# Performance work log

Measured on AMD Instinct MI355X. Metric: run time of the kernel, lower is better.

The kernel has to match this reference:

```python
import jax, jax.numpy as jnp
from jax import lax
import numpy as np

B, S, D = 64, 512, 768
W = 256          # number of words per sentence (counts sum <= S since counts in {1,2})
H = 384          # lstm_dim
C = 425          # n_classes


def setup_inputs() -> dict:
    key = jax.random.key(0)
    ks = jax.random.split(key, 12)
    sc_ih = 1.0 / np.sqrt(D)
    sc_hh = 1.0 / np.sqrt(H)
    return {
        "f0": jax.random.normal(ks[0], (B, S, D), dtype=jnp.float32),
        "counts": jax.random.randint(ks[1], (B, W), 1, 3, dtype=jnp.int32),  # pieces per word in {1,2}
        "Wih_f": jax.random.normal(ks[2], (4 * H, D), dtype=jnp.float32) * sc_ih,
        "Whh_f": jax.random.normal(ks[3], (4 * H, H), dtype=jnp.float32) * sc_hh,
        "bih_f": jax.random.normal(ks[4], (4 * H,), dtype=jnp.float32) * sc_hh,
        "bhh_f": jax.random.normal(ks[5], (4 * H,), dtype=jnp.float32) * sc_hh,
        "Wih_b": jax.random.normal(ks[6], (4 * H, D), dtype=jnp.float32) * sc_ih,
        "Whh_b": jax.random.normal(ks[7], (4 * H, H), dtype=jnp.float32) * sc_hh,
        "bih_b": jax.random.normal(ks[8], (4 * H,), dtype=jnp.float32) * sc_hh,
        "bhh_b": jax.random.normal(ks[9], (4 * H,), dtype=jnp.float32) * sc_hh,
        "Wlin": jax.random.normal(ks[10], (C, 2 * H), dtype=jnp.float32) * (1.0 / np.sqrt(2 * H)),
        "blin": jax.random.normal(ks[11], (C,), dtype=jnp.float32) * 0.02,
    }


def segment_mean_pool(f0, counts):
    # Ragged segment-mean: word j in sentence i pools wordpieces [start, start+counts) .
    starts = jnp.cumsum(counts, axis=1) - counts          # [B, W] start offset per word
    total = jnp.sum(counts, axis=1)                       # [B] total wordpieces used
    pos = jnp.arange(S)
    # segment id of each wordpiece position: number of starts <= pos, minus 1
    seg = jnp.sum(starts[:, :, None] <= pos[None, None, :], axis=1) - 1   # [B, S]
    valid = pos[None, :] < total[:, None]
    seg = jnp.where(valid, seg, W)                        # route padding into dump segment W
    sums = jax.vmap(lambda f, s: jax.ops.segment_sum(f, s, num_segments=W + 1))(f0, seg)  # [B, W+1, D]
    pooled = sums[:, :W] / counts[..., None].astype(f0.dtype)
    # Original writes means into positions [0, W) in-place; tail [W, S) keeps raw states.
    return f0.at[:, :W].set(pooled)


def lstm_dir(x, Wih, Whh, bih, bhh, reverse):
    # x: [B, S, D]; PyTorch gate order i, f, g, o
    xp = jnp.einsum('bsd,gd->bsg', x, Wih) + bih + bhh    # precompute input projections

    def step(carry, xt):
        h, c = carry
        gates = xt + h @ Whh.T
        i, f, g, o = jnp.split(gates, 4, axis=-1)
        c = jax.nn.sigmoid(f) * c + jax.nn.sigmoid(i) * jnp.tanh(g)
        h = jax.nn.sigmoid(o) * jnp.tanh(c)
        return (h, c), h

    init = (jnp.zeros((x.shape[0], H), x.dtype), jnp.zeros((x.shape[0], H), x.dtype))
    _, hs = lax.scan(step, init, jnp.swapaxes(xp, 0, 1), reverse=reverse)  # [S, B, H]
    return jnp.swapaxes(hs, 0, 1)


def reference(f0, counts, Wih_f, Whh_f, bih_f, bhh_f, Wih_b, Whh_b, bih_b, bhh_b, Wlin, blin):
    f0 = segment_mean_pool(f0, counts)
    hf = lstm_dir(f0, Wih_f, Whh_f, bih_f, bhh_f, reverse=False)
    hb = lstm_dir(f0, Wih_b, Whh_b, bih_b, bhh_b, reverse=True)
    f1 = jnp.concatenate([hf, hb], axis=-1)               # [B, S, 2H]
    # Linear then dropout (eval mode -> identity)
    return jnp.einsum('bsh,ch->bsc', f1, Wlin) + blin
```

## Files before the change

### kernel.cpp

```cpp
#include <hip/hip_runtime.h>
#include <stdint.h>


typedef __attribute__((ext_vector_type(8))) short short8;
typedef __attribute__((ext_vector_type(4))) float f32x4;

static constexpr int Bn = 64, Sn = 512, Dn = 768, Wn = 256, Hn = 384, Cn = 425;
static constexpr int G4H = 4 * Hn;
static constexpr int NBT = 4;
static constexpr int NCK = 6;

__device__ __forceinline__ unsigned short f2bf(float f) {
  unsigned int u = __float_as_uint(f);
  u += 0x7FFFu + ((u >> 16) & 1u);
  return (unsigned short)(u >> 16);
}
__device__ __forceinline__ float bf2f(unsigned short h) {
  return __uint_as_float(((unsigned int)h) << 16);
}
__device__ __forceinline__ float sigm(float x)  { return 1.f / (1.f + __expf(-x)); }
__device__ __forceinline__ float tanhft(float x){ return 1.f - 2.f / (__expf(2.f * x) + 1.f); }

#define GLL16(gp, lp) __builtin_amdgcn_global_load_lds( \
  (const __attribute__((address_space(1))) unsigned int*)(gp), \
  (__attribute__((address_space(3))) unsigned int*)(lp), 16, 0, 0)

__global__ void zero_comm(unsigned int* p, int nwords) {
  int i = blockIdx.x * 256 + threadIdx.x;
  if (i < nwords)
    __hip_atomic_store(&p[i], 0u, __ATOMIC_RELAXED, __HIP_MEMORY_SCOPE_AGENT);
}

__global__ void scan_starts(const int* __restrict__ counts, int* __restrict__ starts) {
  int b = blockIdx.x, j = threadIdx.x;
  __shared__ int sm[256];
  int c = counts[b * Wn + j];
  sm[j] = c;
  __syncthreads();
  for (int off = 1; off < 256; off <<= 1) {
    int v = (j >= off) ? sm[j - off] : 0;
    __syncthreads();
    sm[j] += v;
    __syncthreads();
  }
  starts[b * Wn + j] = sm[j] - c;
}

__global__ void prep_cast(const float* __restrict__ Wih_f, const float* __restrict__ Wih_b,
                          const float* __restrict__ Whh_f, const float* __restrict__ Whh_b,
                          const float* __restrict__ Wlin,
                          const float* __restrict__ bih_f, const float* __restrict__ bhh_f,
                          const float* __restrict__ bih_b, const float* __restrict__ bhh_b,
                          unsigned short* __restrict__ wih, unsigned short* __restrict__ whh,
                          unsigned short* __restrict__ wlin, float* __restrict__ biasc) {
  int i = blockIdx.x * 256 + threadIdx.x;
  const int T0 = 3072 * 768;
  const int T1 = 2 * 1536 * 384;
  const int T2 = Cn * 768;
  const int T3 = 3072;
  if (i < T0) {
    int n = i / 768, k = i - n * 768;
    float v = (n < 1536) ? Wih_f[n * 768 + k] : Wih_b[(n - 1536) * 768 + k];
    wih[i] = f2bf(v);
  } else if (i < T0 + T1) {
    int j = i - T0;
    float v = (j < 1536 * 384) ? Whh_f[j] : Whh_b[j - 1536 * 384];
    whh[j] = f2bf(v);
  } else if (i < T0 + T1 + T2) {
    int j = i - T0 - T1;
    wlin[j] = f2bf(Wlin[j]);
  } else if (i < T0 + T1 + T2 + T3) {
    int n = i - T0 - T1 - T2;
    biasc[n] = (n < 1536) ? (bih_f[n] + bhh_f[n]) : (bih_b[n - 1536] + bhh_b[n - 1536]);
  }
}

__global__ void pool_kernel(const float* __restrict__ f0, const int* __restrict__ counts,
                            const int* __restrict__ starts, unsigned short* __restrict__ f0p) {
  int idx = blockIdx.x * 256 + threadIdx.x;
  int dc = idx % 192;
  int rest = idx / 192;
  int s = rest & 511, b = rest >> 9;
  const float4* f4 = (const float4*)f0;
  float4 v;
  if (s < Wn) {
    int st = starts[b * Wn + s], cnt = counts[b * Wn + s];
    v = f4[(size_t)(b * Sn + st) * 192 + dc];
    if (cnt == 2) {
      float4 v2 = f4[(size_t)(b * Sn + st + 1) * 192 + dc];
      v.x = (v.x + v2.x) * 0.5f; v.y = (v.y + v2.y) * 0.5f;
      v.z = (v.z + v2.z) * 0.5f; v.w = (v.w + v2.w) * 0.5f;
    }
  } else {
    v = f4[(size_t)(b * Sn + s) * 192 + dc];
  }
  ushort4 o;
  o.x = f2bf(v.x); o.y = f2bf(v.y); o.z = f2bf(v.z); o.w = f2bf(v.w);
  ((ushort4*)f0p)[(size_t)(b * Sn + s) * 192 + dc] = o;
}

__global__ void gemm_xp(const unsigned short* __restrict__ A, const unsigned short* __restrict__ Bw,
                        const float* __restrict__ biasc, unsigned short* __restrict__ xp) {
  __shared__ __align__(16) unsigned short As[128 * 32];
  __shared__ __align__(16) unsigned short Bs[128 * 32];
  int tid = threadIdx.x, w = tid >> 6, l = tid & 63, lr = l & 15, lq = l >> 4;
  int mBase = blockIdx.x * 128, nBase = blockIdx.y * 128;
  int mw = (w & 1) * 64, nw = (w >> 1) * 64;
  f32x4 acc[4][4];
#pragma unroll
  for (int mt = 0; mt < 4; ++mt)
#pragma unroll
    for (int nt = 0; nt < 4; ++nt) acc[mt][nt] = (f32x4){0.f, 0.f, 0.f, 0.f};

  for (int kb = 0; kb < 24; ++kb) {
    int k0 = kb * 32;
#pragma unroll
    for (int j = 0; j < 2; ++j) {
      int g = j * 256 + tid;
      int row = g >> 2, kc = (g & 3) * 8;
      GLL16(A + (size_t)(mBase + row) * 768 + k0 + kc, (char*)As + (j * 256 + w * 64) * 16);
      GLL16(Bw + (size_t)(nBase + row) * 768 + k0 + kc, (char*)Bs + (j * 256 + w * 64) * 16);
    }
    __syncthreads();
    short8 af[4], bfv[4];
#pragma unroll
    for (int mt = 0; mt < 4; ++mt) af[mt] = *(const short8*)&As[(mw + mt * 16 + lr) * 32 + lq * 8];
#pragma unroll
    for (int nt = 0; nt < 4; ++nt) bfv[nt] = *(const short8*)&Bs[(nw + nt * 16 + lr) * 32 + lq * 8];
#pragma unroll
    for (int mt = 0; mt < 4; ++mt)
#pragma unroll
      for (int nt = 0; nt < 4; ++nt)
        acc[mt][nt] = __builtin_amdgcn_mfma_f32_16x16x32_bf16(af[mt], bfv[nt], acc[mt][nt], 0, 0, 0);
    __syncthreads();
  }
#pragma unroll
  for (int nt = 0; nt < 4; ++nt) {
    int n = nBase + nw + nt * 16 + lr;
    float bias = biasc[n];
    int d = (n >= 1536) ? 1 : 0;
    int gI = n - d * 1536;
#pragma unroll
    for (int mt = 0; mt < 4; ++mt) {
      int mrow = mBase + mw + mt * 16 + lq * 4;
#pragma unroll
      for (int r = 0; r < 4; ++r) {
        int m = mrow + r;
        int t = m & 511, b = m >> 9;
        xp[((size_t)((d * Sn + t) * Bn + b)) * 1536 + gI] = f2bf(acc[mt][nt][r] + bias);
      }
    }
  }
}

__global__ void __launch_bounds__(256, 1)
recur_kernel(const unsigned short* __restrict__ whh,
             const unsigned short* __restrict__ xp,
             unsigned short* __restrict__ h_all,
             unsigned int* __restrict__ htag) {
  int bid = blockIdx.x;
  int dir = bid / (NBT * NCK);
  int rem = bid % (NBT * NCK);
  int btile = rem / NCK, chunk = rem % NCK;
  int tid = threadIdx.x, w = tid >> 6, l = tid & 63, lr = l & 15, lq = l >> 4;
  int hwb = chunk * 64 + w * 16;
  int pr = tid >> 4, pk = tid & 15;

  __shared__ __align__(16) unsigned int hlds[2][16 * 196];

  short8 bfr[4][12];
#pragma unroll
  for (int q = 0; q < 4; ++q)
#pragma unroll
    for (int kf = 0; kf < 12; ++kf)
      bfr[q][kf] = *(const short8*)&whh[((size_t)dir * 1536 + q * 384 + hwb + lr) * 384 + kf * 32 + lq * 8];

  f32x4 c0 = (f32x4){0.f, 0.f, 0.f, 0.f};

  for (int it = 0; it < Sn; ++it) {
    int t = dir ? (Sn - 1 - it) : it;

    f32x4 acc[4];
#pragma unroll
    for (int q = 0; q < 4; ++q) {
#pragma unroll
      for (int r = 0; r < 4; ++r) {
        int b = btile * 16 + lq * 4 + r;
        acc[q][r] = bf2f(xp[((size_t)((dir * Sn + t) * Bn + b)) * 1536 + q * 384 + hwb + lr]);
      }
    }

    if (it > 0) {
      const unsigned int expT = (unsigned int)it;
      int slot = (it - 1) & 1;
      const unsigned long long* srow = (const unsigned long long*)
          (htag + (size_t)(dir * 2 + slot) * 64 * 384 + (size_t)(btile * 16 + pr) * 384);
      unsigned long long v[12];
      while (true) {
        bool ok = true;
#pragma unroll
        for (int i = 0; i < 12; ++i) {
          unsigned long long x = __hip_atomic_load(&srow[pk + 16 * i],
                                   __ATOMIC_RELAXED, __HIP_MEMORY_SCOPE_AGENT);
          v[i] = x;
          ok &= (((unsigned int)(x >> 16) & 0xffffu) == expT) &
                ((unsigned int)(x >> 48) == expT);
        }
        if (__all((int)ok)) break;
        __builtin_amdgcn_s_sleep(1);
      }
      unsigned int* dst = hlds[it & 1];
#pragma unroll
      for (int i = 0; i < 12; ++i)
        dst[pr * 196 + pk + 16 * i] = ((unsigned int)v[i] & 0xffffu) |
                                      (((unsigned int)(v[i] >> 32) & 0xffffu) << 16);
      __syncthreads();
      const char* src = (const char*)hlds[it & 1];
#pragma unroll
      for (int kf = 0; kf < 12; ++kf) {
        short8 a = *(const short8*)(src + lr * 784 + kf * 64 + lq * 16);
#pragma unroll
        for (int q = 0; q < 4; ++q)
          acc[q] = __builtin_amdgcn_mfma_f32_16x16x32_bf16(a, bfr[q][kf], acc[q], 0, 0, 0);
      }
    }

    unsigned int outTag = (unsigned int)(it + 1) << 16;
    int oslot = it & 1;
    unsigned int* obase = htag + (size_t)(dir * 2 + oslot) * 64 * 384;
    unsigned short hb16v[4];
#pragma unroll
    for (int r = 0; r < 4; ++r) {
      float iv = sigm(acc[0][r]);
      float fv = sigm(acc[1][r]);
      float gv = tanhft(acc[2][r]);
      float ov = sigm(acc[3][r]);
      float cf = fv * c0[r] + iv * gv;
      c0[r] = cf;
      float hv = ov * tanhft(cf);
      hb16v[r] = f2bf(hv);
      int b = btile * 16 + lq * 4 + r;
      __hip_atomic_store(&obase[(size_t)b * 384 + hwb + lr],
                         outTag | hb16v[r], __ATOMIC_RELAXED, __HIP_MEMORY_SCOPE_AGENT);
    }
#pragma unroll
    for (int r = 0; r < 4; ++r) {
      int b = btile * 16 + lq * 4 + r;
      h_all[((size_t)b * Sn + t) * 768 + dir * Hn + hwb + lr] = hb16v[r];
    }
  }
}

__global__ void gemm_out(const unsigned short* __restrict__ A, const unsigned short* __restrict__ Bw,
                         const float* __restrict__ blin, float* __restrict__ out) {
  __shared__ __align__(16) unsigned short As[128 * 32];
  __shared__ __align__(16) unsigned short Bs[128 * 32];
  int tid = threadIdx.x, w = tid >> 6, l = tid & 63, lr = l & 15, lq = l >> 4;
  int mBase = blockIdx.x * 128, nBase = blockIdx.y * 128;
  int mw = (w & 1) * 64, nw = (w >> 1) * 64;
  f32x4 acc[4][4];
#pragma unroll
  for (int mt = 0; mt < 4; ++mt)
#pragma unroll
    for (int nt = 0; nt < 4; ++nt) acc[mt][nt] = (f32x4){0.f, 0.f, 0.f, 0.f};

  for (int kb = 0; kb < 24; ++kb) {
    int k0 = kb * 32;
#pragma unroll
    for (int j = 0; j < 2; ++j) {
      int g = j * 256 + tid;
      int row = g >> 2, kc = (g & 3) * 8;
      int nr = nBase + row; if (nr > Cn - 1) nr = Cn - 1;
      GLL16(A + (size_t)(mBase + row) * 768 + k0 + kc, (char*)As + (j * 256 + w * 64) * 16);
      GLL16(Bw + (size_t)nr * 768 + k0 + kc, (char*)Bs + (j * 256 + w * 64) * 16);
    }
    __syncthreads();
    short8 af[4], bfv[4];
#pragma unroll
    for (int mt = 0; mt < 4; ++mt) af[mt] = *(const short8*)&As[(mw + mt * 16 + lr) * 32 + lq * 8];
#pragma unroll
    for (int nt = 0; nt < 4; ++nt) bfv[nt] = *(const short8*)&Bs[(nw + nt * 16 + lr) * 32 + lq * 8];
#pragma unroll
    for (int mt = 0; mt < 4; ++mt)
#pragma unroll
      for (int nt = 0; nt < 4; ++nt)
        acc[mt][nt] = __builtin_amdgcn_mfma_f32_16x16x32_bf16(af[mt], bfv[nt], acc[mt][nt], 0, 0, 0);
    __syncthreads();
  }
#pragma unroll
  for (int nt = 0; nt < 4; ++nt) {
    int n = nBase + nw + nt * 16 + lr;
    if (n < Cn) {
      float bias = blin[n];
#pragma unroll
      for (int mt = 0; mt < 4; ++mt) {
        int mrow = mBase + mw + mt * 16 + lq * 4;
#pragma unroll
        for (int r = 0; r < 4; ++r) {
          int m = mrow + r;
          out[(size_t)m * Cn + n] = acc[mt][nt][r] + bias;
        }
      }
    }
  }
}

extern "C" void kernel_launch(void* const* d_in, const int* in_sizes, int n_in,
                              void* d_out, int out_size, void* d_ws, size_t ws_size,
                              hipStream_t stream) {
  (void)in_sizes; (void)n_in; (void)out_size;
  const float* f0     = (const float*)d_in[0];
  const int*   counts = (const int*)  d_in[1];
  const float* Wih_f  = (const float*)d_in[2];
  const float* Whh_f  = (const float*)d_in[3];
  const float* bih_f  = (const float*)d_in[4];
  const float* bhh_f  = (const float*)d_in[5];
  const float* Wih_b  = (const float*)d_in[6];
  const float* Whh_b  = (const float*)d_in[7];
  const float* bih_b  = (const float*)d_in[8];
  const float* bhh_b  = (const float*)d_in[9];
  const float* Wlin   = (const float*)d_in[10];
  const float* blin   = (const float*)d_in[11];
  float* out = (float*)d_out;

  char* ws = (char*)d_ws;
  size_t o = 0;
  auto alloc = [&](size_t bytes) { size_t cur = o; o += (bytes + 255) & ~(size_t)255; return cur; };
  size_t o_f0p    = alloc((size_t)Bn * Sn * Dn * 2);
  size_t o_xp     = alloc((size_t)2 * Sn * Bn * G4H * 2);
  size_t o_wih    = alloc((size_t)3072 * 768 * 2);
  size_t o_whh    = alloc((size_t)2 * 1536 * 384 * 2);
  size_t o_wlin   = alloc((size_t)Cn * 768 * 2);
  size_t o_bias   = alloc((size_t)3072 * 4);
  size_t o_starts = alloc((size_t)Bn * Wn * 4);
  size_t o_htag   = alloc((size_t)2 * 2 * 64 * 384 * 4);
  if (o > ws_size) return;

  unsigned short* f0p   = (unsigned short*)(ws + o_f0p);
  unsigned short* h_all = (unsigned short*)(ws + o_f0p);
  unsigned short* xp    = (unsigned short*)(ws + o_xp);
  unsigned short* wih   = (unsigned short*)(ws + o_wih);
  unsigned short* whh   = (unsigned short*)(ws + o_whh);
  unsigned short* wlin  = (unsigned short*)(ws + o_wlin);
  float*          biasc = (float*)(ws + o_bias);
  int*            starts= (int*)(ws + o_starts);
  unsigned int*   htag  = (unsigned int*)(ws + o_htag);

  {
    int nwords = 2 * 2 * 64 * 384;
    zero_comm<<<(nwords + 255) / 256, 256, 0, stream>>>(htag, nwords);
  }
  scan_starts<<<Bn, 256, 0, stream>>>(counts, starts);
  {
    int total = 3072 * 768 + 2 * 1536 * 384 + Cn * 768 + 3072;
    prep_cast<<<(total + 255) / 256, 256, 0, stream>>>(Wih_f, Wih_b, Whh_f, Whh_b, Wlin,
                                                       bih_f, bhh_f, bih_b, bhh_b,
                                                       wih, whh, wlin, biasc);
  }
  pool_kernel<<<(Bn * Sn * 192) / 256, 256, 0, stream>>>(f0, counts, starts, f0p);
  gemm_xp<<<dim3(256, 24), 256, 0, stream>>>(f0p, wih, biasc, xp);
  recur_kernel<<<2 * NBT * NCK, 256, 0, stream>>>(whh, xp, h_all, htag);
  gemm_out<<<dim3(256, 4), 256, 0, stream>>>(h_all, wlin, blin, out);
}
```

Baseline: 1.889 ms.

## Exchange LSTM hidden state through XCD-local buffers with runtime XCD detection

The recurrence kernel now launches 64 blocks and maps them so that each group of six chunk-blocks sharing a batch tile and direction can detect whether they all landed on the same XCD. When they did, hidden states are exchanged through a per-XCD buffer using sc0 loads and stores, so the polling traffic can stay in the XCD-local cache instead of going to device-coherent memory. A bounded spin falls back to the original agent-scope tagged buffer, which is still always written. The change also prefetches the next step's input projections into registers to hide load latency, and swizzles the LDS layout to reduce bank conflicts. The XCD-local path relies on the hardware scheduler's block-to-XCD placement and on cache-coherence behaviour. It adds setup handshakes and duplicate stores.

```diff
diff --git a/kernel.cpp b/kernel.cpp
--- a/kernel.cpp
+++ b/kernel.cpp
@@ -4,11 +4,13 @@
 
 typedef __attribute__((ext_vector_type(8))) short short8;
 typedef __attribute__((ext_vector_type(4))) float f32x4;
+typedef __attribute__((ext_vector_type(4))) unsigned int u32x4;
 
 static constexpr int Bn = 64, Sn = 512, Dn = 768, Wn = 256, Hn = 384, Cn = 425;
 static constexpr int G4H = 4 * Hn;
 static constexpr int NBT = 4;
 static constexpr int NCK = 6;
+static constexpr int REGW = 2 * 16 * 384;
 
 __device__ __forceinline__ unsigned short f2bf(float f) {
   unsigned int u = __float_as_uint(f);
@@ -157,15 +159,71 @@
 recur_kernel(const unsigned short* __restrict__ whh,
              const unsigned short* __restrict__ xp,
              unsigned short* __restrict__ h_all,
-             unsigned int* __restrict__ htag) {
+             unsigned int* __restrict__ htag,
+             unsigned int* __restrict__ htagF,
+             unsigned int* __restrict__ xcdtab) {
   int bid = blockIdx.x;
-  int dir = bid / (NBT * NCK);
-  int rem = bid % (NBT * NCK);
-  int btile = rem / NCK, chunk = rem % NCK;
+  int k = bid & 7, j = bid >> 3;
+  if (j >= NCK) return;
+  int dir = k >> 2, btile = k & 3, chunk = j;
   int tid = threadIdx.x, w = tid >> 6, l = tid & 63, lr = l & 15, lq = l >> 4;
   int hwb = chunk * 64 + w * 16;
   int pr = tid >> 4, pk = tid & 15;
 
+  unsigned int xcdr;
+  asm volatile("s_getreg_b32 %0, hwreg(HW_REG_XCC_ID)" : "=s"(xcdr));
+  int myx = (int)(xcdr & 7u);
+  __shared__ int sh_fast;
+  if (tid == 0) {
+    __hip_atomic_store(&xcdtab[k * 8 + chunk], (unsigned)(myx | 0x10),
+                       __ATOMIC_RELAXED, __HIP_MEMORY_SCOPE_AGENT);
+    unsigned int first = 0; bool una = true;
+    for (int j2 = 0; j2 < NCK; ++j2) {
+      unsigned int u;
+      while (!(u = __hip_atomic_load(&xcdtab[k * 8 + j2], __ATOMIC_RELAXED,
+                                     __HIP_MEMORY_SCOPE_AGENT)))
+        __builtin_amdgcn_s_sleep(1);
+      if (j2 == 0) first = u; else una = una && (u == first);
+    }
+    int f = 0;
+    if (una) {
+      if (chunk == 0) {
+        unsigned int exp0 = 0;
+        __hip_atomic_compare_exchange_strong(&xcdtab[128 + myx], &exp0, (unsigned)(k + 1),
+            __ATOMIC_RELAXED, __ATOMIC_RELAXED, __HIP_MEMORY_SCOPE_AGENT);
+      }
+      unsigned int cl;
+      while (!(cl = __hip_atomic_load(&xcdtab[128 + myx], __ATOMIC_RELAXED,
+                                      __HIP_MEMORY_SCOPE_AGENT)))
+        __builtin_amdgcn_s_sleep(1);
+      f = (cl == (unsigned)(k + 1)) ? 1 : 0;
+    }
+    sh_fast = f;
+  }
+  __syncthreads();
+  const bool fast = (sh_fast != 0);
+  unsigned int* regF = htagF + (size_t)myx * REGW;
+
+  if (fast) {
+    u32x4 z4 = (u32x4){0u, 0u, 0u, 0u};
+    unsigned int* p0 = regF + tid * 48;
+#pragma unroll
+    for (int i = 0; i < 12; ++i)
+      asm volatile("global_store_dwordx4 %0, %1, off sc0"
+                   :: "v"(p0 + i * 4), "v"(z4) : "memory");
+    asm volatile("s_waitcnt vmcnt(0)" ::: "memory");
+    __syncthreads();
+    if (tid == 0) {
+      __hip_atomic_store(&xcdtab[64 + k * 8 + chunk], 1u, __ATOMIC_RELAXED,
+                         __HIP_MEMORY_SCOPE_AGENT);
+      for (int j2 = 0; j2 < NCK; ++j2)
+        while (!__hip_atomic_load(&xcdtab[64 + k * 8 + j2], __ATOMIC_RELAXED,
+                                  __HIP_MEMORY_SCOPE_AGENT))
+          __builtin_amdgcn_s_sleep(1);
+    }
+    __syncthreads();
+  }
+
   __shared__ __align__(16) unsigned int hlds[2][16 * 196];
 
   short8 bfr[4][12];
@@ -175,50 +233,101 @@
     for (int kf = 0; kf < 12; ++kf)
       bfr[q][kf] = *(const short8*)&whh[((size_t)dir * 1536 + q * 384 + hwb + lr) * 384 + kf * 32 + lq * 8];
 
+  auto ldxp = [&](int tt, unsigned short* dst) {
+#pragma unroll
+    for (int q = 0; q < 4; ++q)
+#pragma unroll
+      for (int r = 0; r < 4; ++r) {
+        int b = btile * 16 + lq * 4 + r;
+        dst[q * 4 + r] = xp[((size_t)((dir * Sn + tt) * Bn + b)) * 1536 + q * 384 + hwb + lr];
+      }
+  };
+  unsigned short xcur[16], xnxt[16];
+  ldxp(dir ? (Sn - 1) : 0, xcur);
+
   f32x4 c0 = (f32x4){0.f, 0.f, 0.f, 0.f};
+  bool fastc = fast;
 
   for (int it = 0; it < Sn; ++it) {
     int t = dir ? (Sn - 1 - it) : it;
+    int tn = (it + 1 < Sn) ? (dir ? (Sn - 2 - it) : (it + 1)) : t;
+    ldxp(tn, xnxt);
 
     f32x4 acc[4];
 #pragma unroll
-    for (int q = 0; q < 4; ++q) {
-#pragma unroll
-      for (int r = 0; r < 4; ++r) {
-        int b = btile * 16 + lq * 4 + r;
-        acc[q][r] = bf2f(xp[((size_t)((dir * Sn + t) * Bn + b)) * 1536 + q * 384 + hwb + lr]);
-      }
-    }
+    for (int q = 0; q < 4; ++q) acc[q] = (f32x4){0.f, 0.f, 0.f, 0.f};
 
     if (it > 0) {
       const unsigned int expT = (unsigned int)it;
       int slot = (it - 1) & 1;
-      const unsigned long long* srow = (const unsigned long long*)
-          (htag + (size_t)(dir * 2 + slot) * 64 * 384 + (size_t)(btile * 16 + pr) * 384);
       unsigned long long v[12];
-      while (true) {
-        bool ok = true;
-#pragma unroll
-        for (int i = 0; i < 12; ++i) {
-          unsigned long long x = __hip_atomic_load(&srow[pk + 16 * i],
-                                   __ATOMIC_RELAXED, __HIP_MEMORY_SCOPE_AGENT);
-          v[i] = x;
-          ok &= (((unsigned int)(x >> 16) & 0xffffu) == expT) &
-                ((unsigned int)(x >> 48) == expT);
+      bool have = false;
+      if (fastc) {
+        const unsigned long long* srowF = (const unsigned long long*)
+            (regF + (size_t)slot * 6144 + (size_t)pr * 384);
+        const void* sp = (const void*)(srowF + pk);
+        int rounds = 0;
+        while (true) {
+          unsigned long long a0, a1, a2, a3, a4, a5, a6, a7, a8, a9, a10, a11;
+          asm volatile(
+            "global_load_dwordx2 %0,  %12, off sc0\n\t"
+            "global_load_dwordx2 %1,  %12, off offset:128 sc0\n\t"
+            "global_load_dwordx2 %2,  %12, off offset:256 sc0\n\t"
+            "global_load_dwordx2 %3,  %12, off offset:384 sc0\n\t"
+            "global_load_dwordx2 %4,  %12, off offset:512 sc0\n\t"
+            "global_load_dwordx2 %5,  %12, off offset:640 sc0\n\t"
+            "global_load_dwordx2 %6,  %12, off offset:768 sc0\n\t"
+            "global_load_dwordx2 %7,  %12, off offset:896 sc0\n\t"
+            "global_load_dwordx2 %8,  %12, off offset:1024 sc0\n\t"
+            "global_load_dwordx2 %9,  %12, off offset:1152 sc0\n\t"
+            "global_load_dwordx2 %10, %12, off offset:1280 sc0\n\t"
+            "global_load_dwordx2 %11, %12, off offset:1408 sc0\n\t"
+            "s_waitcnt vmcnt(0)"
+            : "=&v"(a0), "=&v"(a1), "=&v"(a2), "=&v"(a3), "=&v"(a4), "=&v"(a5),
+              "=&v"(a6), "=&v"(a7), "=&v"(a8), "=&v"(a9), "=&v"(a10), "=&v"(a11)
+            : "v"(sp)
+            : "memory");
+          v[0] = a0; v[1] = a1; v[2] = a2; v[3] = a3; v[4] = a4; v[5] = a5;
+          v[6] = a6; v[7] = a7; v[8] = a8; v[9] = a9; v[10] = a10; v[11] = a11;
+          bool ok = true;
+#pragma unroll
+          for (int i = 0; i < 12; ++i)
+            ok &= (((unsigned int)(v[i] >> 16) & 0xffffu) == expT) &
+                  ((unsigned int)(v[i] >> 48) == expT);
+          if (__all((int)ok)) { have = true; break; }
+          if (++rounds > 4096) { fastc = false; break; }
+          __builtin_amdgcn_s_sleep(1);
         }
-        if (__all((int)ok)) break;
-        __builtin_amdgcn_s_sleep(1);
+      }
+      if (!have) {
+        const unsigned long long* srow = (const unsigned long long*)
+            (htag + (size_t)(dir * 2 + slot) * 64 * 384 + (size_t)(btile * 16 + pr) * 384);
+        while (true) {
+          bool ok = true;
+#pragma unroll
+          for (int i = 0; i < 12; ++i) {
+            unsigned long long x = __hip_atomic_load(&srow[pk + 16 * i],
+                                     __ATOMIC_RELAXED, __HIP_MEMORY_SCOPE_AGENT);
+            v[i] = x;
+            ok &= (((unsigned int)(x >> 16) & 0xffffu) == expT) &
+                  ((unsigned int)(x >> 48) == expT);
+          }
+          if (__all((int)ok)) break;
+          __builtin_amdgcn_s_sleep(1);
+        }
       }
       unsigned int* dst = hlds[it & 1];
 #pragma unroll
       for (int i = 0; i < 12; ++i)
-        dst[pr * 196 + pk + 16 * i] = ((unsigned int)v[i] & 0xffffu) |
-                                      (((unsigned int)(v[i] >> 32) & 0xffffu) << 16);
+        dst[pr * 196 + ((pk + 16 * i) ^ ((pr & 7) << 2))] =
+            ((unsigned int)v[i] & 0xffffu) |
+            (((unsigned int)(v[i] >> 32) & 0xffffu) << 16);
       __syncthreads();
       const char* src = (const char*)hlds[it & 1];
 #pragma unroll
       for (int kf = 0; kf < 12; ++kf) {
-        short8 a = *(const short8*)(src + lr * 784 + kf * 64 + lq * 16);
+        short8 a = *(const short8*)(src + lr * 784 +
+                                    ((kf * 64 + lq * 16) ^ ((lr & 7) << 4)));
 #pragma unroll
         for (int q = 0; q < 4; ++q)
           acc[q] = __builtin_amdgcn_mfma_f32_16x16x32_bf16(a, bfr[q][kf], acc[q], 0, 0, 0);
@@ -228,26 +337,34 @@
     unsigned int outTag = (unsigned int)(it + 1) << 16;
     int oslot = it & 1;
     unsigned int* obase = htag + (size_t)(dir * 2 + oslot) * 64 * 384;
+    unsigned int* obF = regF + (size_t)oslot * 6144;
     unsigned short hb16v[4];
 #pragma unroll
     for (int r = 0; r < 4; ++r) {
-      float iv = sigm(acc[0][r]);
-      float fv = sigm(acc[1][r]);
-      float gv = tanhft(acc[2][r]);
-      float ov = sigm(acc[3][r]);
+      float iv = sigm(acc[0][r] + bf2f(xcur[0 * 4 + r]));
+      float fv = sigm(acc[1][r] + bf2f(xcur[1 * 4 + r]));
+      float gv = tanhft(acc[2][r] + bf2f(xcur[2 * 4 + r]));
+      float ov = sigm(acc[3][r] + bf2f(xcur[3 * 4 + r]));
       float cf = fv * c0[r] + iv * gv;
       c0[r] = cf;
       float hv = ov * tanhft(cf);
       hb16v[r] = f2bf(hv);
+      unsigned int val = outTag | hb16v[r];
+      if (fast) {
+        unsigned int* pF = obF + (size_t)(lq * 4 + r) * 384 + hwb + lr;
+        asm volatile("global_store_dword %0, %1, off sc0" :: "v"(pF), "v"(val) : "memory");
+      }
       int b = btile * 16 + lq * 4 + r;
-      __hip_atomic_store(&obase[(size_t)b * 384 + hwb + lr],
-                         outTag | hb16v[r], __ATOMIC_RELAXED, __HIP_MEMORY_SCOPE_AGENT);
+      __hip_atomic_store(&obase[(size_t)b * 384 + hwb + lr], val,
+                         __ATOMIC_RELAXED, __HIP_MEMORY_SCOPE_AGENT);
     }
 #pragma unroll
     for (int r = 0; r < 4; ++r) {
       int b = btile * 16 + lq * 4 + r;
       h_all[((size_t)b * Sn + t) * 768 + dir * Hn + hwb + lr] = hb16v[r];
     }
+#pragma unroll
+    for (int i = 0; i < 16; ++i) xcur[i] = xnxt[i];
   }
 }
 
@@ -334,6 +451,8 @@
   size_t o_bias   = alloc((size_t)3072 * 4);
   size_t o_starts = alloc((size_t)Bn * Wn * 4);
   size_t o_htag   = alloc((size_t)2 * 2 * 64 * 384 * 4);
+  size_t o_xcds   = alloc((size_t)160 * 4);
+  size_t o_htagF  = alloc((size_t)8 * REGW * 4);
   if (o > ws_size) return;
 
   unsigned short* f0p   = (unsigned short*)(ws + o_f0p);
@@ -345,9 +464,11 @@
   float*          biasc = (float*)(ws + o_bias);
   int*            starts= (int*)(ws + o_starts);
   unsigned int*   htag  = (unsigned int*)(ws + o_htag);
+  unsigned int*   xcdtab= (unsigned int*)(ws + o_xcds);
+  unsigned int*   htagF = (unsigned int*)(ws + o_htagF);
 
   {
-    int nwords = 2 * 2 * 64 * 384;
+    int nwords = 2 * 2 * 64 * 384 + 160;
     zero_comm<<<(nwords + 255) / 256, 256, 0, stream>>>(htag, nwords);
   }
   scan_starts<<<Bn, 256, 0, stream>>>(counts, starts);
@@ -359,6 +480,6 @@
   }
   pool_kernel<<<(Bn * Sn * 192) / 256, 256, 0, stream>>>(f0, counts, starts, f0p);
   gemm_xp<<<dim3(256, 24), 256, 0, stream>>>(f0p, wih, biasc, xp);
-  recur_kernel<<<2 * NBT * NCK, 256, 0, stream>>>(whh, xp, h_all, htag);
+  recur_kernel<<<64, 256, 0, stream>>>(whh, xp, h_all, htag, htagF, xcdtab);
   gemm_out<<<dim3(256, 4), 256, 0, stream>>>(h_all, wlin, blin, out);
 }
```

New measurement: 6.944 ms. 268% more time.

## Fuse input-projection GEMM with LSTM recurrence using per-timestep-group readiness counters

Applied to the files above, without the earlier changes.

The separate gemm_xp and recur_kernel launches become one kernel. The first 48 blocks run the recurrence, and the remaining blocks compute input-projection tiles in time order from both sequence ends, each bumping a group counter when done. Recurrence blocks spin on these counters before loading xp, and they prefetch the next step's xp while the current step's MFMA runs. Activations switch to a time-major layout so each GEMM tile covers whole timesteps, with matching index changes in pool_kernel and gemm_out. The aim is to hide the projection GEMM behind the serial recurrence. The cost is added spin-wait synchronisation and reliance on the recurrence blocks being resident together to avoid deadlock.

```diff
diff --git a/kernel.cpp b/kernel.cpp
--- a/kernel.cpp
+++ b/kernel.cpp
@@ -9,6 +9,7 @@
 static constexpr int G4H = 4 * Hn;
 static constexpr int NBT = 4;
 static constexpr int NCK = 6;
+static constexpr int NRWG = 2 * NBT * NCK;
 
 __device__ __forceinline__ unsigned short f2bf(float f) {
   unsigned int u = __float_as_uint(f);
@@ -96,15 +97,143 @@
   }
   ushort4 o;
   o.x = f2bf(v.x); o.y = f2bf(v.y); o.z = f2bf(v.z); o.w = f2bf(v.w);
-  ((ushort4*)f0p)[(size_t)(b * Sn + s) * 192 + dc] = o;
-}
-
-__global__ void gemm_xp(const unsigned short* __restrict__ A, const unsigned short* __restrict__ Bw,
-                        const float* __restrict__ biasc, unsigned short* __restrict__ xp) {
-  __shared__ __align__(16) unsigned short As[128 * 32];
-  __shared__ __align__(16) unsigned short Bs[128 * 32];
+  ((ushort4*)f0p)[(size_t)(s * Bn + b) * 192 + dc] = o;
+}
+
+__global__ void __launch_bounds__(256, 1)
+fused_kernel(const unsigned short* __restrict__ whh,
+             unsigned short* xp,
+             unsigned short* f0h,
+             const unsigned short* __restrict__ wih,
+             const float* __restrict__ biasc,
+             unsigned int* htag,
+             unsigned int* gcnt) {
+  __shared__ __align__(16) char smem[25088];
+  int bid = blockIdx.x;
   int tid = threadIdx.x, w = tid >> 6, l = tid & 63, lr = l & 15, lq = l >> 4;
-  int mBase = blockIdx.x * 128, nBase = blockIdx.y * 128;
+
+  if (bid < NRWG) {
+    int dir = bid / (NBT * NCK);
+    int rem = bid % (NBT * NCK);
+    int btile = rem / NCK, chunk = rem % NCK;
+    int hwb = chunk * 64 + w * 16;
+    int pr = tid >> 4, pk = tid & 15;
+    unsigned int (*hlds)[16 * 196] = (unsigned int (*)[16 * 196])smem;
+
+    short8 bfr[4][12];
+#pragma unroll
+    for (int q = 0; q < 4; ++q)
+#pragma unroll
+      for (int kf = 0; kf < 12; ++kf)
+        bfr[q][kf] = *(const short8*)&whh[((size_t)dir * 1536 + q * 384 + hwb + lr) * 384 + kf * 32 + lq * 8];
+
+    int lastG = -1;
+    auto gate = [&](int tt) {
+      int g = tt >> 4;
+      if (g != lastG) {
+        while (__hip_atomic_load(&gcnt[g], __ATOMIC_RELAXED, __HIP_MEMORY_SCOPE_AGENT) < 192u)
+          __builtin_amdgcn_s_sleep(4);
+        lastG = g;
+        asm volatile("" ::: "memory");
+      }
+    };
+    auto ldxp = [&](int tt, unsigned short* dst) {
+#pragma unroll
+      for (int q = 0; q < 4; ++q)
+#pragma unroll
+        for (int r = 0; r < 4; ++r) {
+          int b = btile * 16 + lq * 4 + r;
+          dst[q * 4 + r] = xp[((size_t)((dir * Sn + tt) * Bn + b)) * 1536 + q * 384 + hwb + lr];
+        }
+    };
+    unsigned short xcur[16], xnxt[16];
+    int t0 = dir ? (Sn - 1) : 0;
+    gate(t0);
+    ldxp(t0, xcur);
+
+    f32x4 c0 = (f32x4){0.f, 0.f, 0.f, 0.f};
+
+    for (int it = 0; it < Sn; ++it) {
+      int t = dir ? (Sn - 1 - it) : it;
+      int tn = (it + 1 < Sn) ? (dir ? (Sn - 2 - it) : (it + 1)) : t;
+      gate(tn);
+      ldxp(tn, xnxt);
+
+      f32x4 acc[4];
+#pragma unroll
+      for (int q = 0; q < 4; ++q) acc[q] = (f32x4){0.f, 0.f, 0.f, 0.f};
+
+      if (it > 0) {
+        const unsigned int expT = (unsigned int)it;
+        int slot = (it - 1) & 1;
+        const unsigned long long* srow = (const unsigned long long*)
+            (htag + (size_t)(dir * 2 + slot) * 64 * 384 + (size_t)(btile * 16 + pr) * 384);
+        unsigned long long v[12];
+        while (true) {
+          bool ok = true;
+#pragma unroll
+          for (int i = 0; i < 12; ++i) {
+            unsigned long long x = __hip_atomic_load(&srow[pk + 16 * i],
+                                     __ATOMIC_RELAXED, __HIP_MEMORY_SCOPE_AGENT);
+            v[i] = x;
+            ok &= (((unsigned int)(x >> 16) & 0xffffu) == expT) &
+                  ((unsigned int)(x >> 48) == expT);
+          }
+          if (__all((int)ok)) break;
+          __builtin_amdgcn_s_sleep(1);
+        }
+        unsigned int* dst = hlds[it & 1];
+#pragma unroll
+        for (int i = 0; i < 12; ++i)
+          dst[pr * 196 + pk + 16 * i] = ((unsigned int)v[i] & 0xffffu) |
+                                        (((unsigned int)(v[i] >> 32) & 0xffffu) << 16);
+        __syncthreads();
+        const char* src = (const char*)hlds[it & 1];
+#pragma unroll
+        for (int kf = 0; kf < 12; ++kf) {
+          short8 a = *(const short8*)(src + lr * 784 + kf * 64 + lq * 16);
+#pragma unroll
+          for (int q = 0; q < 4; ++q)
+            acc[q] = __builtin_amdgcn_mfma_f32_16x16x32_bf16(a, bfr[q][kf], acc[q], 0, 0, 0);
+        }
+      }
+
+      unsigned int outTag = (unsigned int)(it + 1) << 16;
+      int oslot = it & 1;
+      unsigned int* obase = htag + (size_t)(dir * 2 + oslot) * 64 * 384;
+      unsigned short hb16v[4];
+#pragma unroll
+      for (int r = 0; r < 4; ++r) {
+        float iv = sigm(acc[0][r] + bf2f(xcur[0 * 4 + r]));
+        float fv = sigm(acc[1][r] + bf2f(xcur[1 * 4 + r]));
+        float gv = tanhft(acc[2][r] + bf2f(xcur[2 * 4 + r]));
+        float ov = sigm(acc[3][r] + bf2f(xcur[3 * 4 + r]));
+        float cf = fv * c0[r] + iv * gv;
+        c0[r] = cf;
+        float hv = ov * tanhft(cf);
+        hb16v[r] = f2bf(hv);
+        int b = btile * 16 + lq * 4 + r;
+        __hip_atomic_store(&obase[(size_t)b * 384 + hwb + lr],
+                           outTag | hb16v[r], __ATOMIC_RELAXED, __HIP_MEMORY_SCOPE_AGENT);
+      }
+#pragma unroll
+      for (int r = 0; r < 4; ++r) {
+        int b = btile * 16 + lq * 4 + r;
+        f0h[((size_t)(t * Bn + b)) * 768 + dir * Hn + hwb + lr] = hb16v[r];
+      }
+#pragma unroll
+      for (int i = 0; i < 16; ++i) xcur[i] = xnxt[i];
+    }
+    return;
+  }
+
+  int gb = bid - NRWG;
+  int q = gb / 48, r = gb % 48;
+  int mtile = (r < 24) ? q : (255 - q);
+  int ntile = r % 24;
+  unsigned short* As = (unsigned short*)smem;
+  unsigned short* Bs = (unsigned short*)(smem + 8192);
+  int mBase = mtile * 128, nBase = ntile * 128;
   int mw = (w & 1) * 64, nw = (w >> 1) * 64;
   f32x4 acc[4][4];
 #pragma unroll
@@ -118,8 +247,8 @@
     for (int j = 0; j < 2; ++j) {
       int g = j * 256 + tid;
       int row = g >> 2, kc = (g & 3) * 8;
-      GLL16(A + (size_t)(mBase + row) * 768 + k0 + kc, (char*)As + (j * 256 + w * 64) * 16);
-      GLL16(Bw + (size_t)(nBase + row) * 768 + k0 + kc, (char*)Bs + (j * 256 + w * 64) * 16);
+      GLL16(f0h + (size_t)(mBase + row) * 768 + k0 + kc, (char*)As + (j * 256 + w * 64) * 16);
+      GLL16(wih + (size_t)(nBase + row) * 768 + k0 + kc, (char*)Bs + (j * 256 + w * 64) * 16);
     }
     __syncthreads();
     short8 af[4], bfv[4];
@@ -135,120 +264,27 @@
     __syncthreads();
   }
 #pragma unroll
-  for (int nt = 0; nt < 4; ++nt) {
-    int n = nBase + nw + nt * 16 + lr;
-    float bias = biasc[n];
-    int d = (n >= 1536) ? 1 : 0;
-    int gI = n - d * 1536;
-#pragma unroll
-    for (int mt = 0; mt < 4; ++mt) {
-      int mrow = mBase + mw + mt * 16 + lq * 4;
-#pragma unroll
-      for (int r = 0; r < 4; ++r) {
-        int m = mrow + r;
-        int t = m & 511, b = m >> 9;
-        xp[((size_t)((d * Sn + t) * Bn + b)) * 1536 + gI] = f2bf(acc[mt][nt][r] + bias);
-      }
-    }
-  }
-}
-
-__global__ void __launch_bounds__(256, 1)
-recur_kernel(const unsigned short* __restrict__ whh,
-             const unsigned short* __restrict__ xp,
-             unsigned short* __restrict__ h_all,
-             unsigned int* __restrict__ htag) {
-  int bid = blockIdx.x;
-  int dir = bid / (NBT * NCK);
-  int rem = bid % (NBT * NCK);
-  int btile = rem / NCK, chunk = rem % NCK;
-  int tid = threadIdx.x, w = tid >> 6, l = tid & 63, lr = l & 15, lq = l >> 4;
-  int hwb = chunk * 64 + w * 16;
-  int pr = tid >> 4, pk = tid & 15;
-
-  __shared__ __align__(16) unsigned int hlds[2][16 * 196];
-
-  short8 bfr[4][12];
-#pragma unroll
-  for (int q = 0; q < 4; ++q)
-#pragma unroll
-    for (int kf = 0; kf < 12; ++kf)
-      bfr[q][kf] = *(const short8*)&whh[((size_t)dir * 1536 + q * 384 + hwb + lr) * 384 + kf * 32 + lq * 8];
-
-  f32x4 c0 = (f32x4){0.f, 0.f, 0.f, 0.f};
-
-  for (int it = 0; it < Sn; ++it) {
-    int t = dir ? (Sn - 1 - it) : it;
-
-    f32x4 acc[4];
-#pragma unroll
-    for (int q = 0; q < 4; ++q) {
-#pragma unroll
-      for (int r = 0; r < 4; ++r) {
-        int b = btile * 16 + lq * 4 + r;
-        acc[q][r] = bf2f(xp[((size_t)((dir * Sn + t) * Bn + b)) * 1536 + q * 384 + hwb + lr]);
-      }
-    }
-
-    if (it > 0) {
-      const unsigned int expT = (unsigned int)it;
-      int slot = (it - 1) & 1;
-      const unsigned long long* srow = (const unsigned long long*)
-          (htag + (size_t)(dir * 2 + slot) * 64 * 384 + (size_t)(btile * 16 + pr) * 384);
-      unsigned long long v[12];
-      while (true) {
-        bool ok = true;
-#pragma unroll
-        for (int i = 0; i < 12; ++i) {
-          unsigned long long x = __hip_atomic_load(&srow[pk + 16 * i],
-                                   __ATOMIC_RELAXED, __HIP_MEMORY_SCOPE_AGENT);
-          v[i] = x;
-          ok &= (((unsigned int)(x >> 16) & 0xffffu) == expT) &
-                ((unsigned int)(x >> 48) == expT);
-        }
-        if (__all((int)ok)) break;
-        __builtin_amdgcn_s_sleep(1);
-      }
-      unsigned int* dst = hlds[it & 1];
-#pragma unroll
-      for (int i = 0; i < 12; ++i)
-        dst[pr * 196 + pk + 16 * i] = ((unsigned int)v[i] & 0xffffu) |
-                                      (((unsigned int)(v[i] >> 32) & 0xffffu) << 16);
-      __syncthreads();
-      const char* src = (const char*)hlds[it & 1];
-#pragma unroll
-      for (int kf = 0; kf < 12; ++kf) {
-        short8 a = *(const short8*)(src + lr * 784 + kf * 64 + lq * 16);
-#pragma unroll
-        for (int q = 0; q < 4; ++q)
-          acc[q] = __builtin_amdgcn_mfma_f32_16x16x32_bf16(a, bfr[q][kf], acc[q], 0, 0, 0);
-      }
-    }
-
-    unsigned int outTag = (unsigned int)(it + 1) << 16;
-    int oslot = it & 1;
-    unsigned int* obase = htag + (size_t)(dir * 2 + oslot) * 64 * 384;
-    unsigned short hb16v[4];
-#pragma unroll
-    for (int r = 0; r < 4; ++r) {
-      float iv = sigm(acc[0][r]);
-      float fv = sigm(acc[1][r]);
-      float gv = tanhft(acc[2][r]);
-      float ov = sigm(acc[3][r]);
-      float cf = fv * c0[r] + iv * gv;
-      c0[r] = cf;
-      float hv = ov * tanhft(cf);
-      hb16v[r] = f2bf(hv);
-      int b = btile * 16 + lq * 4 + r;
-      __hip_atomic_store(&obase[(size_t)b * 384 + hwb + lr],
-                         outTag | hb16v[r], __ATOMIC_RELAXED, __HIP_MEMORY_SCOPE_AGENT);
-    }
-#pragma unroll
-    for (int r = 0; r < 4; ++r) {
-      int b = btile * 16 + lq * 4 + r;
-      h_all[((size_t)b * Sn + t) * 768 + dir * Hn + hwb + lr] = hb16v[r];
-    }
-  }
+  for (int mt = 0; mt < 4; ++mt) {
+#pragma unroll
+    for (int rr = 0; rr < 4; ++rr) {
+      int m = mBase + mw + mt * 16 + lq * 4 + rr;
+      int t = m >> 6, b = m & 63;
+#pragma unroll
+      for (int nt = 0; nt < 4; ++nt) {
+        int n = nBase + nw + nt * 16 + lr;
+        int d = (n >= 1536) ? 1 : 0;
+        int gI = n - d * 1536;
+        unsigned short val = f2bf(acc[mt][nt][rr] + biasc[n]);
+        __hip_atomic_store(&xp[((size_t)((d * Sn + t) * Bn + b)) * 1536 + gI], val,
+                           __ATOMIC_RELAXED, __HIP_MEMORY_SCOPE_AGENT);
+      }
+    }
+  }
+  asm volatile("s_waitcnt vmcnt(0)" ::: "memory");
+  __syncthreads();
+  if (tid == 0)
+    __hip_atomic_fetch_add(&gcnt[mtile >> 3], 1u, __ATOMIC_RELAXED,
+                           __HIP_MEMORY_SCOPE_AGENT);
 }
 
 __global__ void gemm_out(const unsigned short* __restrict__ A, const unsigned short* __restrict__ Bw,
@@ -294,11 +330,11 @@
       float bias = blin[n];
 #pragma unroll
       for (int mt = 0; mt < 4; ++mt) {
-        int mrow = mBase + mw + mt * 16 + lq * 4;
 #pragma unroll
         for (int r = 0; r < 4; ++r) {
-          int m = mrow + r;
-          out[(size_t)m * Cn + n] = acc[mt][nt][r] + bias;
+          int m = mBase + mw + mt * 16 + lq * 4 + r;
+          int t = m >> 6, b = m & 63;
+          out[((size_t)(b * Sn + t)) * Cn + n] = acc[mt][nt][r] + bias;
         }
       }
     }
@@ -334,10 +370,10 @@
   size_t o_bias   = alloc((size_t)3072 * 4);
   size_t o_starts = alloc((size_t)Bn * Wn * 4);
   size_t o_htag   = alloc((size_t)2 * 2 * 64 * 384 * 4);
+  size_t o_gcnt   = alloc((size_t)32 * 4);
   if (o > ws_size) return;
 
-  unsigned short* f0p   = (unsigned short*)(ws + o_f0p);
-  unsigned short* h_all = (unsigned short*)(ws + o_f0p);
+  unsigned short* f0h   = (unsigned short*)(ws + o_f0p);
   unsigned short* xp    = (unsigned short*)(ws + o_xp);
   unsigned short* wih   = (unsigned short*)(ws + o_wih);
   unsigned short* whh   = (unsigned short*)(ws + o_whh);
@@ -345,9 +381,10 @@
   float*          biasc = (float*)(ws + o_bias);
   int*            starts= (int*)(ws + o_starts);
   unsigned int*   htag  = (unsigned int*)(ws + o_htag);
+  unsigned int*   gcnt  = (unsigned int*)(ws + o_gcnt);
 
   {
-    int nwords = 2 * 2 * 64 * 384;
+    int nwords = 2 * 2 * 64 * 384 + 32;
     zero_comm<<<(nwords + 255) / 256, 256, 0, stream>>>(htag, nwords);
   }
   scan_starts<<<Bn, 256, 0, stream>>>(counts, starts);
@@ -357,8 +394,7 @@
                                                        bih_f, bhh_f, bih_b, bhh_b,
                                                        wih, whh, wlin, biasc);
   }
-  pool_kernel<<<(Bn * Sn * 192) / 256, 256, 0, stream>>>(f0, counts, starts, f0p);
-  gemm_xp<<<dim3(256, 24), 256, 0, stream>>>(f0p, wih, biasc, xp);
-  recur_kernel<<<2 * NBT * NCK, 256, 0, stream>>>(whh, xp, h_all, htag);
-  gemm_out<<<dim3(256, 4), 256, 0, stream>>>(h_all, wlin, blin, out);
-}
+  pool_kernel<<<(Bn * Sn * 192) / 256, 256, 0, stream>>>(f0, counts, starts, f0h);
+  fused_kernel<<<NRWG + 6144, 256, 0, stream>>>(whh, xp, f0h, wih, biasc, htag, gcnt);
+  gemm_out<<<dim3(256, 4), 256, 0, stream>>>(f0h, wlin, blin, out);
+}
```

Result: no change. 1.902 ms (+0.7%).
